# Kernel optimization log

Measured on AMD Instinct MI355X. Metric: run time of the kernel, lower is better.

Reference implementation:

```python
import jax, jax.numpy as jnp
import numpy as np

# Structural constants (CSG module-level globals)
S, N = 250, 200            # sequences, peds per sequence (uniform for vectorization)
MAX = 16                   # MAX_CONSIDERED_PED
H, E = 64, 64              # h_dim, EMBEDDING_DIM
HID, BN = 512, 32          # mlp_pre_pool hidden, BOTTLENECK_DIM


def setup_inputs() -> dict:
    key = jax.random.key(0)
    ks = jax.random.split(key, 8)
    g = lambda k, shape, s=0.05: jax.random.normal(k, shape, dtype=jnp.float32) * s
    h_states = jax.random.normal(ks[0], (S * N, H), dtype=jnp.float32)
    last_pos = jax.random.normal(ks[1], (S * N, 2), dtype=jnp.float32) * 5.0
    starts = np.arange(S, dtype=np.int64) * N
    seq_start_end = jnp.asarray(np.stack([starts, starts + N], axis=1))
    return {
        "h_states": h_states,
        "last_pos": last_pos,
        "W_pos": g(ks[2], (2, E)), "b_pos": jnp.zeros((E,), jnp.float32),
        "W1": g(ks[3], (H + E, HID)), "b1": jnp.zeros((HID,), jnp.float32),
        "W2": g(ks[4], (HID, BN)), "b2": jnp.zeros((BN,), jnp.float32),
        "W_attn": g(ks[5], (MAX * BN, MAX)), "b_attn": jnp.zeros((MAX,), jnp.float32),
        "seq_start_end": seq_start_end,
        "train_or_test": 0,
    }


def reference(h_states, last_pos, W_pos, b_pos, W1, b1, W2, b2, W_attn, b_attn,
              seq_start_end, train_or_test):
    h = h_states.reshape(S, N, H)          # per-sequence hidden states
    pos = last_pos.reshape(S, N, 2)
    # social_features[s, i, j] = pos[s, j] - pos[s, i]
    rel = pos[:, None, :, :] - pos[:, :, None, :]          # [S, N, N, 2]
    # pairwise distances only feed argsort -> stop_gradient (avoids sqrt(0) NaN in vjp)
    dist = jnp.linalg.norm(jax.lax.stop_gradient(rel), axis=-1)  # [S, N, N]
    idx = jnp.argsort(dist, axis=-1)
    # original torch code sorts rows by the attached idx-value column then truncates:
    # this selects rows j with idx[s,i,j] < MAX, i.e. the inverse permutation prefix
    sel = jnp.argsort(idx, axis=-1)[..., :MAX]             # [S, N, MAX]
    # gather neighbor hidden states and relative positions
    h_sel = jax.vmap(lambda hh, ss: hh[ss])(h, sel)        # [S, N, MAX, H]
    feat_sel = jnp.take_along_axis(rel, sel[..., None], axis=2)  # [S, N, MAX, 2]
    emb = feat_sel @ W_pos + b_pos                         # pos_embedding, [S,N,MAX,E]
    x = jnp.concatenate([h_sel, emb], axis=-1)             # [S, N, MAX, H+E]
    # mlp_pre_pool: Linear->ReLU, Linear->ReLU (batch_norm off, dropout 0)
    x = jax.nn.relu(x @ W1 + b1)                           # [S, N, MAX, HID]
    x = jax.nn.relu(x @ W2 + b2)                           # [S, N, MAX, BN]
    logits = x.reshape(S, N, MAX * BN) @ W_attn + b_attn   # [S, N, MAX]
    w = jax.nn.softmax(logits, axis=-1)
    out = jnp.sum(x * w[..., None], axis=2)                # attention-weighted pool
    return out.reshape(S * N, BN)
```

## Files before the change

### kernel.cpp

```cpp
#include <hip/hip_runtime.h>
#include <hip/hip_bf16.h>

#define S_CNT 250
#define N_PED 200
#define MAXP  16
#define HID   512
#define BN    32

#define WS1_FRAGS 8192
#define WS2_FRAGS 2048
#define WS_NEED   163840u

typedef __attribute__((ext_vector_type(8))) short short8;
typedef __attribute__((ext_vector_type(4))) float floatx4;

__device__ __forceinline__ short f2bu(float f) {
    union { __hip_bfloat16 h; unsigned short u; } c;
    c.h = __float2bfloat16(f);
    return (short)c.u;
}

__global__ __launch_bounds__(256) void cvt_kernel(
    const float* __restrict__ W1, const float* __restrict__ W2,
    short8* __restrict__ ws1, short8* __restrict__ ws2)
{
    int t = blockIdx.x * 256 + threadIdx.x;
    if (t < WS1_FRAGS) {
        int lane = t & 63, ks = (t >> 6) & 3, nt = (t >> 8) & 3, pass = t >> 10;
        int n  = pass * 64 + nt * 16 + (lane & 15);
        int k0 = ks * 32 + ((lane >> 4) << 3);
        short8 v;
#pragma unroll
        for (int j = 0; j < 8; ++j) v[j] = f2bu(W1[(k0 + j) * HID + n]);
        ws1[t] = v;
    } else if (t < WS1_FRAGS + WS2_FRAGS) {
        int t2 = t - WS1_FRAGS;
        int lane = t2 & 63, nt2 = (t2 >> 6) & 1, kcl = (t2 >> 7) & 1, pass = t2 >> 8;
        int kc = pass * 2 + kcl;
        int n  = nt2 * 16 + (lane & 15);
        int k0 = kc * 32 + ((lane >> 4) << 3);
        short8 v;
#pragma unroll
        for (int j = 0; j < 8; ++j) v[j] = f2bu(W2[(k0 + j) * BN + n]);
        ws2[t2] = v;
    }
}

__global__ __launch_bounds__(256, 2) void fused_pre(
    const float* __restrict__ h_states, const float* __restrict__ last_pos,
    const float* __restrict__ Wpos,     const float* __restrict__ bpos,
    const float* __restrict__ b1,       const float* __restrict__ b2,
    const float* __restrict__ Wa,       const float* __restrict__ ba,
    const short8* __restrict__ ws1,     const short8* __restrict__ ws2,
    float* __restrict__ out)
{
    __shared__ unsigned short X1c[4][2][16][42];
    __shared__ float X2s[4][512];
    __shared__ float px[N_PED], py[N_PED];
    __shared__ float LG[4][16], WS[4][16];

    const int tid = threadIdx.x;
    const int wv  = tid >> 6;
    const int ln  = tid & 63;
    const int q8  = (ln >> 4) << 3;
    const int c15 = ln & 15;
    const int s    = blockIdx.x / 25;
    const int base = s * N_PED;
    const int il0  = (blockIdx.x % 25) * 8 + wv * 2;

    if (tid < N_PED) {
        px[tid] = last_pos[(base + tid) * 2 + 0];
        py[tid] = last_pos[(base + tid) * 2 + 1];
    }
    __syncthreads();

    short8  af[2][4];
    floatx4 c2[2][2] = {};
    for (int pedi = 0; pedi < 2; ++pedi) {
        const int il = il0 + pedi;
        const float xi = px[il], yi = py[il];
        const int mm = c15, qq = ln >> 4;
        int cnt;
        {
            float dxm = __fsub_rn(px[mm], xi), dym = __fsub_rn(py[mm], yi);
            float dm = __fsqrt_rn(__builtin_fmaf(dxm, dxm, __fmul_rn(dym, dym)));
            cnt = 0;
            for (int j = qq * 50; j < qq * 50 + 50; ++j) {
                float dx = __fsub_rn(px[j], xi), dy = __fsub_rn(py[j], yi);
                float dj = __fsqrt_rn(__builtin_fmaf(dx, dx, __fmul_rn(dy, dy)));
                cnt += (dj < dm || (dj == dm && j < mm)) ? 1 : 0;
            }
            cnt += __shfl_xor(cnt, 16, 64);
            cnt += __shfl_xor(cnt, 32, 64);
        }
        const int sm = cnt;
#pragma unroll
        for (int ks = 0; ks < 2; ++ks) {
            const float* hp = &h_states[(base + sm) * 64 + ks * 32 + q8];
            short8 v;
#pragma unroll
            for (int j = 0; j < 8; ++j) v[j] = f2bu(hp[j]);
            af[pedi][ks] = v;
        }
        const float fx = px[sm] - xi, fy = py[sm] - yi;
#pragma unroll
        for (int ks = 2; ks < 4; ++ks) {
            int e0 = (ks - 2) * 32 + q8;
            short8 v;
#pragma unroll
            for (int j = 0; j < 8; ++j) {
                float e = fx * Wpos[e0 + j] + fy * Wpos[64 + e0 + j] + bpos[e0 + j];
                v[j] = f2bu(e);
            }
            af[pedi][ks] = v;
        }
    }

    for (int p = 0; p < 8; ++p) {
#pragma unroll
        for (int ntl = 0; ntl < 4; ++ntl) {
            const int nt = p * 4 + ntl;
            short8 bf[4];
#pragma unroll
            for (int ks = 0; ks < 4; ++ks)
                bf[ks] = ws1[p * 1024 + ntl * 256 + ks * 64 + ln];
            const float bb = b1[nt * 16 + c15];
            const int colb = (ntl & 1) * 16 + c15;
#pragma unroll
            for (int pedi = 0; pedi < 2; ++pedi) {
                floatx4 c = {};
#pragma unroll
                for (int ks = 0; ks < 4; ++ks)
                    c = __builtin_amdgcn_mfma_f32_16x16x32_bf16(
                            af[pedi][ks], bf[ks], c, 0, 0, 0);
#pragma unroll
                for (int r = 0; r < 4; ++r)
                    X1c[wv][pedi][(ln >> 4) * 4 + r][colb] =
                        (unsigned short)f2bu(fmaxf(c[r] + bb, 0.f));
            }
            if (ntl & 1) {
                const int kcl = ntl >> 1;
                short8 w20 = ws2[p * 256 + kcl * 128 + ln];
                short8 w21 = ws2[p * 256 + kcl * 128 + 64 + ln];
#pragma unroll
                for (int pedi = 0; pedi < 2; ++pedi) {
                    short8 a2 = *(const short8*)&X1c[wv][pedi][c15][q8];
                    c2[pedi][0] = __builtin_amdgcn_mfma_f32_16x16x32_bf16(
                            a2, w20, c2[pedi][0], 0, 0, 0);
                    c2[pedi][1] = __builtin_amdgcn_mfma_f32_16x16x32_bf16(
                            a2, w21, c2[pedi][1], 0, 0, 0);
                }
            }
        }
    }

    for (int pedi = 0; pedi < 2; ++pedi) {
#pragma unroll
        for (int nt2 = 0; nt2 < 2; ++nt2) {
            const float bb2 = b2[nt2 * 16 + c15];
#pragma unroll
            for (int r = 0; r < 4; ++r)
                X2s[wv][((ln >> 4) * 4 + r) * 32 + nt2 * 16 + c15] =
                    fmaxf(c2[pedi][nt2][r] + bb2, 0.f);
        }
        {
            int t = c15, g = ln >> 4;
            float lg = 0.f;
            for (int k = g * 128; k < g * 128 + 128; ++k)
                lg += X2s[wv][k] * Wa[k * MAXP + t];
            lg += __shfl_xor(lg, 16, 64);
            lg += __shfl_xor(lg, 32, 64);
            if (ln < 16) LG[wv][ln] = lg + ba[ln];
        }
        float mx = -1e30f;
#pragma unroll
        for (int m = 0; m < MAXP; ++m) mx = fmaxf(mx, LG[wv][m]);
        float sum = 0.f;
#pragma unroll
        for (int m = 0; m < MAXP; ++m) sum += expf(LG[wv][m] - mx);
        if (ln < 16) WS[wv][ln] = expf(LG[wv][ln] - mx) / sum;
        if (ln < BN) {
            float o = 0.f;
#pragma unroll
            for (int m = 0; m < MAXP; ++m) o += WS[wv][m] * X2s[wv][m * BN + ln];
            out[(base + il0 + pedi) * BN + ln] = o;
        }
    }
}

__global__ __launch_bounds__(256, 2) void fused_fb(
    const float* __restrict__ h_states, const float* __restrict__ last_pos,
    const float* __restrict__ Wpos,     const float* __restrict__ bpos,
    const float* __restrict__ W1,       const float* __restrict__ b1,
    const float* __restrict__ W2,       const float* __restrict__ b2,
    const float* __restrict__ Wa,       const float* __restrict__ ba,
    float* __restrict__ out)
{
    __shared__ short8 fb1[1024];
    __shared__ short8 fb2[256];
    __shared__ unsigned short X1c[4][16][40];
    __shared__ float X2s[4][512];
    __shared__ float px[N_PED], py[N_PED];
    __shared__ float LG[4][16], WS[4][16];

    const int tid = threadIdx.x;
    const int wv  = tid >> 6;
    const int ln  = tid & 63;
    const int q8  = (ln >> 4) << 3;
    const int c15 = ln & 15;
    const int s    = blockIdx.x / 25;
    const int base = s * N_PED;
    const int il0  = (blockIdx.x % 25) * 8 + wv * 2;

    if (tid < N_PED) {
        px[tid] = last_pos[(base + tid) * 2 + 0];
        py[tid] = last_pos[(base + tid) * 2 + 1];
    }
    __syncthreads();

    short8  af[2][4];
    floatx4 c2[2][2] = {};
    for (int pedi = 0; pedi < 2; ++pedi) {
        const int il = il0 + pedi;
        const float xi = px[il], yi = py[il];
        const int mm = c15, qq = ln >> 4;
        int cnt;
        {
            float dxm = __fsub_rn(px[mm], xi), dym = __fsub_rn(py[mm], yi);
            float dm = __fsqrt_rn(__builtin_fmaf(dxm, dxm, __fmul_rn(dym, dym)));
            cnt = 0;
            for (int j = qq * 50; j < qq * 50 + 50; ++j) {
                float dx = __fsub_rn(px[j], xi), dy = __fsub_rn(py[j], yi);
                float dj = __fsqrt_rn(__builtin_fmaf(dx, dx, __fmul_rn(dy, dy)));
                cnt += (dj < dm || (dj == dm && j < mm)) ? 1 : 0;
            }
            cnt += __shfl_xor(cnt, 16, 64);
            cnt += __shfl_xor(cnt, 32, 64);
        }
        const int sm = cnt;
#pragma unroll
        for (int ks = 0; ks < 2; ++ks) {
            const float* hp = &h_states[(base + sm) * 64 + ks * 32 + q8];
            short8 v;
#pragma unroll
            for (int j = 0; j < 8; ++j) v[j] = f2bu(hp[j]);
            af[pedi][ks] = v;
        }
        const float fx = px[sm] - xi, fy = py[sm] - yi;
#pragma unroll
        for (int ks = 2; ks < 4; ++ks) {
            int e0 = (ks - 2) * 32 + q8;
            short8 v;
#pragma unroll
            for (int j = 0; j < 8; ++j) {
                float e = fx * Wpos[e0 + j] + fy * Wpos[64 + e0 + j] + bpos[e0 + j];
                v[j] = f2bu(e);
            }
            af[pedi][ks] = v;
        }
    }

    for (int p = 0; p < 8; ++p) {
        __syncthreads();
        for (int f = tid; f < 1024; f += 256) {
            int lane = f & 63, ks = (f >> 6) & 3, nt = f >> 8;
            int n  = p * 64 + nt * 16 + (lane & 15);
            int k0 = ks * 32 + ((lane >> 4) << 3);
            short8 v;
#pragma unroll
            for (int j = 0; j < 8; ++j) v[j] = f2bu(W1[(k0 + j) * HID + n]);
            fb1[f] = v;
        }
        {
            int lane = tid & 63, nt2 = (tid >> 6) & 1, kcl = tid >> 7;
            int kc = p * 2 + kcl;
            int n  = nt2 * 16 + (lane & 15);
            int k0 = kc * 32 + ((lane >> 4) << 3);
            short8 v;
#pragma unroll
            for (int j = 0; j < 8; ++j) v[j] = f2bu(W2[(k0 + j) * BN + n]);
            fb2[tid] = v;
        }
        __syncthreads();
#pragma unroll
        for (int pedi = 0; pedi < 2; ++pedi) {
#pragma unroll
            for (int ntl = 0; ntl < 4; ++ntl) {
                const int nt = p * 4 + ntl;
                floatx4 c = {};
#pragma unroll
                for (int ks = 0; ks < 4; ++ks)
                    c = __builtin_amdgcn_mfma_f32_16x16x32_bf16(
                            af[pedi][ks], fb1[ntl * 256 + ks * 64 + ln], c, 0, 0, 0);
                const float bb = b1[nt * 16 + c15];
                const int colb = (ntl & 1) * 16 + c15;
#pragma unroll
                for (int r = 0; r < 4; ++r)
                    X1c[wv][(ln >> 4) * 4 + r][colb] =
                        (unsigned short)f2bu(fmaxf(c[r] + bb, 0.f));
                if (ntl & 1) {
                    const int kcl = ntl >> 1;
                    short8 a2 = *(const short8*)&X1c[wv][c15][q8];
                    c2[pedi][0] = __builtin_amdgcn_mfma_f32_16x16x32_bf16(
                            a2, fb2[kcl * 128 + ln], c2[pedi][0], 0, 0, 0);
                    c2[pedi][1] = __builtin_amdgcn_mfma_f32_16x16x32_bf16(
                            a2, fb2[kcl * 128 + 64 + ln], c2[pedi][1], 0, 0, 0);
                }
            }
        }
    }

    for (int pedi = 0; pedi < 2; ++pedi) {
#pragma unroll
        for (int nt2 = 0; nt2 < 2; ++nt2) {
            const float bb2 = b2[nt2 * 16 + c15];
#pragma unroll
            for (int r = 0; r < 4; ++r)
                X2s[wv][((ln >> 4) * 4 + r) * 32 + nt2 * 16 + c15] =
                    fmaxf(c2[pedi][nt2][r] + bb2, 0.f);
        }
        {
            int t = c15, g = ln >> 4;
            float lg = 0.f;
            for (int k = g * 128; k < g * 128 + 128; ++k)
                lg += X2s[wv][k] * Wa[k * MAXP + t];
            lg += __shfl_xor(lg, 16, 64);
            lg += __shfl_xor(lg, 32, 64);
            if (ln < 16) LG[wv][ln] = lg + ba[ln];
        }
        float mx = -1e30f;
#pragma unroll
        for (int m = 0; m < MAXP; ++m) mx = fmaxf(mx, LG[wv][m]);
        float sum = 0.f;
#pragma unroll
        for (int m = 0; m < MAXP; ++m) sum += expf(LG[wv][m] - mx);
        if (ln < 16) WS[wv][ln] = expf(LG[wv][ln] - mx) / sum;
        if (ln < BN) {
            float o = 0.f;
#pragma unroll
            for (int m = 0; m < MAXP; ++m) o += WS[wv][m] * X2s[wv][m * BN + ln];
            out[(base + il0 + pedi) * BN + ln] = o;
        }
    }
}

extern "C" void kernel_launch(void* const* d_in, const int* in_sizes, int n_in,
                              void* d_out, int out_size, void* d_ws, size_t ws_size,
                              hipStream_t stream) {
    const float* h_states = (const float*)d_in[0];
    const float* last_pos = (const float*)d_in[1];
    const float* Wpos     = (const float*)d_in[2];
    const float* bpos     = (const float*)d_in[3];
    const float* W1       = (const float*)d_in[4];
    const float* b1       = (const float*)d_in[5];
    const float* W2       = (const float*)d_in[6];
    const float* b2       = (const float*)d_in[7];
    const float* Wa       = (const float*)d_in[8];
    const float* ba       = (const float*)d_in[9];

    short8* ws1 = (short8*)d_ws;
    short8* ws2 = ws1 + WS1_FRAGS;
    const int grid = (S_CNT * N_PED) / 8;

    if (ws_size >= WS_NEED) {
        cvt_kernel<<<40, 256, 0, stream>>>(W1, W2, ws1, ws2);
        fused_pre<<<grid, 256, 0, stream>>>(
            h_states, last_pos, Wpos, bpos, b1, b2, Wa, ba, ws1, ws2, (float*)d_out);
    } else {
        fused_fb<<<grid, 256, 0, stream>>>(
            h_states, last_pos, Wpos, bpos, W1, b1, W2, b2, Wa, ba, (float*)d_out);
    }
}
```

Measured before the change: 334.7 us.

## Precompute distances once per ped, transpose attention weights, shuffle-based softmax

The neighbour-rank computation now computes each pairwise distance once into shared memory and counts with vectorized LDS reads, instead of recomputing a sqrt for each of the 16 candidate lanes. The attention weight matrix is transposed in the prep kernel so logits are computed with contiguous float4 loads. Softmax max and sum now use wave shuffles instead of serial LDS reads. This adds a slightly larger workspace and a wave barrier, and uses the fast __expf, which may shift numerics slightly.

```diff
diff --git a/kernel.cpp b/kernel.cpp
--- a/kernel.cpp
+++ b/kernel.cpp
@@ -9,7 +9,8 @@
 
 #define WS1_FRAGS 8192
 #define WS2_FRAGS 2048
-#define WS_NEED   163840u
+#define WAT_QUADS 2048
+#define WS_NEED   196608u
 
 typedef __attribute__((ext_vector_type(8))) short short8;
 typedef __attribute__((ext_vector_type(4))) float floatx4;
@@ -22,7 +23,9 @@
 
 __global__ __launch_bounds__(256) void cvt_kernel(
     const float* __restrict__ W1, const float* __restrict__ W2,
-    short8* __restrict__ ws1, short8* __restrict__ ws2)
+    const float* __restrict__ Wa,
+    short8* __restrict__ ws1, short8* __restrict__ ws2,
+    float* __restrict__ waT)
 {
     int t = blockIdx.x * 256 + threadIdx.x;
     if (t < WS1_FRAGS) {
@@ -43,6 +46,14 @@
 #pragma unroll
         for (int j = 0; j < 8; ++j) v[j] = f2bu(W2[(k0 + j) * BN + n]);
         ws2[t2] = v;
+    } else if (t < WS1_FRAGS + WS2_FRAGS + WAT_QUADS) {
+        int t3 = t - (WS1_FRAGS + WS2_FRAGS);
+        int tt = t3 >> 7;
+        int k0 = (t3 & 127) << 2;
+        floatx4 v;
+#pragma unroll
+        for (int j = 0; j < 4; ++j) v[j] = Wa[(k0 + j) * MAXP + tt];
+        ((floatx4*)waT)[t3] = v;
     }
 }
 
@@ -50,11 +61,179 @@
     const float* __restrict__ h_states, const float* __restrict__ last_pos,
     const float* __restrict__ Wpos,     const float* __restrict__ bpos,
     const float* __restrict__ b1,       const float* __restrict__ b2,
-    const float* __restrict__ Wa,       const float* __restrict__ ba,
+    const float* __restrict__ WaT,      const float* __restrict__ ba,
     const short8* __restrict__ ws1,     const short8* __restrict__ ws2,
     float* __restrict__ out)
 {
     __shared__ unsigned short X1c[4][2][16][42];
+    __shared__ float X2s[4][512];
+    __shared__ float px[N_PED], py[N_PED];
+    __shared__ float WS[4][16];
+
+    const int tid = threadIdx.x;
+    const int wv  = tid >> 6;
+    const int ln  = tid & 63;
+    const int q8  = (ln >> 4) << 3;
+    const int c15 = ln & 15;
+    const int s    = blockIdx.x / 25;
+    const int base = s * N_PED;
+    const int il0  = (blockIdx.x % 25) * 8 + wv * 2;
+
+    if (tid < N_PED) {
+        px[tid] = last_pos[(base + tid) * 2 + 0];
+        py[tid] = last_pos[(base + tid) * 2 + 1];
+    }
+    __syncthreads();
+
+    float* dbuf = (float*)&X2s[wv][0];
+    short8  af[2][4];
+    floatx4 c2[2][2] = {};
+    for (int pedi = 0; pedi < 2; ++pedi) {
+        const int il = il0 + pedi;
+        const float xi = px[il], yi = py[il];
+#pragma unroll
+        for (int j0 = 0; j0 < 256; j0 += 64) {
+            int j = j0 + ln;
+            if (j < N_PED) {
+                float dx = __fsub_rn(px[j], xi), dy = __fsub_rn(py[j], yi);
+                dbuf[j] = __fsqrt_rn(__builtin_fmaf(dx, dx, __fmul_rn(dy, dy)));
+            }
+        }
+        __builtin_amdgcn_wave_barrier();
+        const int mm = c15, qq = ln >> 4;
+        const float dm = dbuf[mm];
+        int cnt = 0;
+        const int jbeg = qq * 48;
+        const int jend = (qq == 3) ? N_PED : (jbeg + 48);
+        for (int j = jbeg; j < jend; j += 4) {
+            floatx4 d4 = *(const floatx4*)&dbuf[j];
+#pragma unroll
+            for (int e = 0; e < 4; ++e)
+                cnt += (d4[e] < dm || (d4[e] == dm && (j + e) < mm)) ? 1 : 0;
+        }
+        cnt += __shfl_xor(cnt, 16, 64);
+        cnt += __shfl_xor(cnt, 32, 64);
+        const int sm = cnt;
+#pragma unroll
+        for (int ks = 0; ks < 2; ++ks) {
+            const float* hp = &h_states[(base + sm) * 64 + ks * 32 + q8];
+            short8 v;
+#pragma unroll
+            for (int j = 0; j < 8; ++j) v[j] = f2bu(hp[j]);
+            af[pedi][ks] = v;
+        }
+        const float fx = px[sm] - xi, fy = py[sm] - yi;
+#pragma unroll
+        for (int ks = 2; ks < 4; ++ks) {
+            int e0 = (ks - 2) * 32 + q8;
+            short8 v;
+#pragma unroll
+            for (int j = 0; j < 8; ++j) {
+                float e = fx * Wpos[e0 + j] + fy * Wpos[64 + e0 + j] + bpos[e0 + j];
+                v[j] = f2bu(e);
+            }
+            af[pedi][ks] = v;
+        }
+    }
+
+    for (int p = 0; p < 8; ++p) {
+#pragma unroll
+        for (int ntl = 0; ntl < 4; ++ntl) {
+            const int nt = p * 4 + ntl;
+            short8 bf[4];
+#pragma unroll
+            for (int ks = 0; ks < 4; ++ks)
+                bf[ks] = ws1[p * 1024 + ntl * 256 + ks * 64 + ln];
+            const float bb = b1[nt * 16 + c15];
+            const int colb = (ntl & 1) * 16 + c15;
+#pragma unroll
+            for (int pedi = 0; pedi < 2; ++pedi) {
+                floatx4 c = {};
+#pragma unroll
+                for (int ks = 0; ks < 4; ++ks)
+                    c = __builtin_amdgcn_mfma_f32_16x16x32_bf16(
+                            af[pedi][ks], bf[ks], c, 0, 0, 0);
+#pragma unroll
+                for (int r = 0; r < 4; ++r)
+                    X1c[wv][pedi][(ln >> 4) * 4 + r][colb] =
+                        (unsigned short)f2bu(fmaxf(c[r] + bb, 0.f));
+            }
+            if (ntl & 1) {
+                const int kcl = ntl >> 1;
+                short8 w20 = ws2[p * 256 + kcl * 128 + ln];
+                short8 w21 = ws2[p * 256 + kcl * 128 + 64 + ln];
+#pragma unroll
+                for (int pedi = 0; pedi < 2; ++pedi) {
+                    short8 a2 = *(const short8*)&X1c[wv][pedi][c15][q8];
+                    c2[pedi][0] = __builtin_amdgcn_mfma_f32_16x16x32_bf16(
+                            a2, w20, c2[pedi][0], 0, 0, 0);
+                    c2[pedi][1] = __builtin_amdgcn_mfma_f32_16x16x32_bf16(
+                            a2, w21, c2[pedi][1], 0, 0, 0);
+                }
+            }
+        }
+    }
+
+    for (int pedi = 0; pedi < 2; ++pedi) {
+#pragma unroll
+        for (int nt2 = 0; nt2 < 2; ++nt2) {
+            const float bb2 = b2[nt2 * 16 + c15];
+#pragma unroll
+            for (int r = 0; r < 4; ++r)
+                X2s[wv][((ln >> 4) * 4 + r) * 32 + nt2 * 16 + c15] =
+                    fmaxf(c2[pedi][nt2][r] + bb2, 0.f);
+        }
+        float lg;
+        {
+            const int t = c15, g = ln >> 4;
+            const float* xr = &X2s[wv][g * 128];
+            const float* wr = WaT + t * 512 + g * 128;
+            lg = 0.f;
+#pragma unroll 8
+            for (int kk = 0; kk < 128; kk += 4) {
+                floatx4 xv = *(const floatx4*)(xr + kk);
+                floatx4 w4 = *(const floatx4*)(wr + kk);
+                lg = __builtin_fmaf(xv[0], w4[0],
+                     __builtin_fmaf(xv[1], w4[1],
+                     __builtin_fmaf(xv[2], w4[2],
+                     __builtin_fmaf(xv[3], w4[3], lg))));
+            }
+            lg += __shfl_xor(lg, 16, 64);
+            lg += __shfl_xor(lg, 32, 64);
+        }
+        const float lgf = lg + ba[c15];
+        float mxv = lgf;
+        mxv = fmaxf(mxv, __shfl_xor(mxv, 1, 64));
+        mxv = fmaxf(mxv, __shfl_xor(mxv, 2, 64));
+        mxv = fmaxf(mxv, __shfl_xor(mxv, 4, 64));
+        mxv = fmaxf(mxv, __shfl_xor(mxv, 8, 64));
+        const float ev = __expf(lgf - mxv);
+        float se = ev;
+        se += __shfl_xor(se, 1, 64);
+        se += __shfl_xor(se, 2, 64);
+        se += __shfl_xor(se, 4, 64);
+        se += __shfl_xor(se, 8, 64);
+        if (ln < 16) WS[wv][ln] = ev / se;
+        if (ln < BN) {
+            float o = 0.f;
+#pragma unroll
+            for (int m = 0; m < MAXP; ++m) o += WS[wv][m] * X2s[wv][m * BN + ln];
+            out[(base + il0 + pedi) * BN + ln] = o;
+        }
+    }
+}
+
+__global__ __launch_bounds__(256, 2) void fused_fb(
+    const float* __restrict__ h_states, const float* __restrict__ last_pos,
+    const float* __restrict__ Wpos,     const float* __restrict__ bpos,
+    const float* __restrict__ W1,       const float* __restrict__ b1,
+    const float* __restrict__ W2,       const float* __restrict__ b2,
+    const float* __restrict__ Wa,       const float* __restrict__ ba,
+    float* __restrict__ out)
+{
+    __shared__ short8 fb1[1024];
+    __shared__ short8 fb2[256];
+    __shared__ unsigned short X1c[4][16][40];
     __shared__ float X2s[4][512];
     __shared__ float px[N_PED], py[N_PED];
     __shared__ float LG[4][16], WS[4][16];
@@ -117,150 +296,6 @@
     }
 
     for (int p = 0; p < 8; ++p) {
-#pragma unroll
-        for (int ntl = 0; ntl < 4; ++ntl) {
-            const int nt = p * 4 + ntl;
-            short8 bf[4];
-#pragma unroll
-            for (int ks = 0; ks < 4; ++ks)
-                bf[ks] = ws1[p * 1024 + ntl * 256 + ks * 64 + ln];
-            const float bb = b1[nt * 16 + c15];
-            const int colb = (ntl & 1) * 16 + c15;
-#pragma unroll
-            for (int pedi = 0; pedi < 2; ++pedi) {
-                floatx4 c = {};
-#pragma unroll
-                for (int ks = 0; ks < 4; ++ks)
-                    c = __builtin_amdgcn_mfma_f32_16x16x32_bf16(
-                            af[pedi][ks], bf[ks], c, 0, 0, 0);
-#pragma unroll
-                for (int r = 0; r < 4; ++r)
-                    X1c[wv][pedi][(ln >> 4) * 4 + r][colb] =
-                        (unsigned short)f2bu(fmaxf(c[r] + bb, 0.f));
-            }
-            if (ntl & 1) {
-                const int kcl = ntl >> 1;
-                short8 w20 = ws2[p * 256 + kcl * 128 + ln];
-                short8 w21 = ws2[p * 256 + kcl * 128 + 64 + ln];
-#pragma unroll
-                for (int pedi = 0; pedi < 2; ++pedi) {
-                    short8 a2 = *(const short8*)&X1c[wv][pedi][c15][q8];
-                    c2[pedi][0] = __builtin_amdgcn_mfma_f32_16x16x32_bf16(
-                            a2, w20, c2[pedi][0], 0, 0, 0);
-                    c2[pedi][1] = __builtin_amdgcn_mfma_f32_16x16x32_bf16(
-                            a2, w21, c2[pedi][1], 0, 0, 0);
-                }
-            }
-        }
-    }
-
-    for (int pedi = 0; pedi < 2; ++pedi) {
-#pragma unroll
-        for (int nt2 = 0; nt2 < 2; ++nt2) {
-            const float bb2 = b2[nt2 * 16 + c15];
-#pragma unroll
-            for (int r = 0; r < 4; ++r)
-                X2s[wv][((ln >> 4) * 4 + r) * 32 + nt2 * 16 + c15] =
-                    fmaxf(c2[pedi][nt2][r] + bb2, 0.f);
-        }
-        {
-            int t = c15, g = ln >> 4;
-            float lg = 0.f;
-            for (int k = g * 128; k < g * 128 + 128; ++k)
-                lg += X2s[wv][k] * Wa[k * MAXP + t];
-            lg += __shfl_xor(lg, 16, 64);
-            lg += __shfl_xor(lg, 32, 64);
-            if (ln < 16) LG[wv][ln] = lg + ba[ln];
-        }
-        float mx = -1e30f;
-#pragma unroll
-        for (int m = 0; m < MAXP; ++m) mx = fmaxf(mx, LG[wv][m]);
-        float sum = 0.f;
-#pragma unroll
-        for (int m = 0; m < MAXP; ++m) sum += expf(LG[wv][m] - mx);
-        if (ln < 16) WS[wv][ln] = expf(LG[wv][ln] - mx) / sum;
-        if (ln < BN) {
-            float o = 0.f;
-#pragma unroll
-            for (int m = 0; m < MAXP; ++m) o += WS[wv][m] * X2s[wv][m * BN + ln];
-            out[(base + il0 + pedi) * BN + ln] = o;
-        }
-    }
-}
-
-__global__ __launch_bounds__(256, 2) void fused_fb(
-    const float* __restrict__ h_states, const float* __restrict__ last_pos,
-    const float* __restrict__ Wpos,     const float* __restrict__ bpos,
-    const float* __restrict__ W1,       const float* __restrict__ b1,
-    const float* __restrict__ W2,       const float* __restrict__ b2,
-    const float* __restrict__ Wa,       const float* __restrict__ ba,
-    float* __restrict__ out)
-{
-    __shared__ short8 fb1[1024];
-    __shared__ short8 fb2[256];
-    __shared__ unsigned short X1c[4][16][40];
-    __shared__ float X2s[4][512];
-    __shared__ float px[N_PED], py[N_PED];
-    __shared__ float LG[4][16], WS[4][16];
-
-    const int tid = threadIdx.x;
-    const int wv  = tid >> 6;
-    const int ln  = tid & 63;
-    const int q8  = (ln >> 4) << 3;
-    const int c15 = ln & 15;
-    const int s    = blockIdx.x / 25;
-    const int base = s * N_PED;
-    const int il0  = (blockIdx.x % 25) * 8 + wv * 2;
-
-    if (tid < N_PED) {
-        px[tid] = last_pos[(base + tid) * 2 + 0];
-        py[tid] = last_pos[(base + tid) * 2 + 1];
-    }
-    __syncthreads();
-
-    short8  af[2][4];
-    floatx4 c2[2][2] = {};
-    for (int pedi = 0; pedi < 2; ++pedi) {
-        const int il = il0 + pedi;
-        const float xi = px[il], yi = py[il];
-        const int mm = c15, qq = ln >> 4;
-        int cnt;
-        {
-            float dxm = __fsub_rn(px[mm], xi), dym = __fsub_rn(py[mm], yi);
-            float dm = __fsqrt_rn(__builtin_fmaf(dxm, dxm, __fmul_rn(dym, dym)));
-            cnt = 0;
-            for (int j = qq * 50; j < qq * 50 + 50; ++j) {
-                float dx = __fsub_rn(px[j], xi), dy = __fsub_rn(py[j], yi);
-                float dj = __fsqrt_rn(__builtin_fmaf(dx, dx, __fmul_rn(dy, dy)));
-                cnt += (dj < dm || (dj == dm && j < mm)) ? 1 : 0;
-            }
-            cnt += __shfl_xor(cnt, 16, 64);
-            cnt += __shfl_xor(cnt, 32, 64);
-        }
-        const int sm = cnt;
-#pragma unroll
-        for (int ks = 0; ks < 2; ++ks) {
-            const float* hp = &h_states[(base + sm) * 64 + ks * 32 + q8];
-            short8 v;
-#pragma unroll
-            for (int j = 0; j < 8; ++j) v[j] = f2bu(hp[j]);
-            af[pedi][ks] = v;
-        }
-        const float fx = px[sm] - xi, fy = py[sm] - yi;
-#pragma unroll
-        for (int ks = 2; ks < 4; ++ks) {
-            int e0 = (ks - 2) * 32 + q8;
-            short8 v;
-#pragma unroll
-            for (int j = 0; j < 8; ++j) {
-                float e = fx * Wpos[e0 + j] + fy * Wpos[64 + e0 + j] + bpos[e0 + j];
-                v[j] = f2bu(e);
-            }
-            af[pedi][ks] = v;
-        }
-    }
-
-    for (int p = 0; p < 8; ++p) {
         __syncthreads();
         for (int f = tid; f < 1024; f += 256) {
             int lane = f & 63, ks = (f >> 6) & 3, nt = f >> 8;
@@ -360,12 +395,13 @@
 
     short8* ws1 = (short8*)d_ws;
     short8* ws2 = ws1 + WS1_FRAGS;
+    float*  waT = (float*)(ws2 + WS2_FRAGS);
     const int grid = (S_CNT * N_PED) / 8;
 
     if (ws_size >= WS_NEED) {
-        cvt_kernel<<<40, 256, 0, stream>>>(W1, W2, ws1, ws2);
+        cvt_kernel<<<48, 256, 0, stream>>>(W1, W2, Wa, ws1, ws2, waT);
         fused_pre<<<grid, 256, 0, stream>>>(
-            h_states, last_pos, Wpos, bpos, b1, b2, Wa, ba, ws1, ws2, (float*)d_out);
+            h_states, last_pos, Wpos, bpos, b1, b2, waT, ba, ws1, ws2, (float*)d_out);
     } else {
         fused_fb<<<grid, 256, 0, stream>>>(
             h_states, last_pos, Wpos, bpos, W1, b1, W2, b2, Wa, ba, (float*)d_out);
```

After: 442.0 us. 1.32x slower.
